# Kernel tuning notes

Measured on AMD Instinct MI355X. Metric: run time of the kernel, lower is better.

## Reference

```python
import jax, jax.numpy as jnp
import numpy as np

N = 50000      # nodes
E = 800000     # edges
IN = 128       # in_channels
H = 128        # hidden_channels
OUT = 500      # out_channels
EPS = 1e-5


def setup_inputs() -> dict:
    key = jax.random.key(0)
    ks = jax.random.split(key, 8)
    def rn(k, shape, scale=0.05):
        return jax.random.normal(k, shape, jnp.float32) * scale
    return {
        "x": jax.random.normal(ks[0], (N, IN), jnp.float32),
        "edge_index": jax.random.randint(ks[1], (2, E), 0, N, dtype=jnp.int32),
        "W1": rn(ks[2], (IN, H)), "b1": jnp.zeros((H,), jnp.float32),
        "g1": jnp.ones((H,), jnp.float32), "be1": jnp.zeros((H,), jnp.float32),
        "W2": rn(ks[3], (H, 2 * H)), "b2": jnp.zeros((2 * H,), jnp.float32),
        "g2": jnp.ones((2 * H,), jnp.float32), "be2": jnp.zeros((2 * H,), jnp.float32),
        "W3": rn(ks[4], (2 * H, H)), "b3": jnp.zeros((H,), jnp.float32),
        "g3": jnp.ones((H,), jnp.float32), "be3": jnp.zeros((H,), jnp.float32),
        "Wl1": rn(ks[5], (H, H // 2)), "bl1": jnp.zeros((H // 2,), jnp.float32),
        "g4": jnp.ones((H // 2,), jnp.float32), "be4": jnp.zeros((H // 2,), jnp.float32),
        "Wl2": rn(ks[6], (H // 2, OUT)), "bl2": jnp.zeros((OUT,), jnp.float32),
    }


def layer_norm(x, g, b):
    mu = jnp.mean(x, axis=-1, keepdims=True)
    var = jnp.mean(jnp.square(x - mu), axis=-1, keepdims=True)
    return (x - mu) * jax.lax.rsqrt(var + EPS) * g + b


def gcn_conv(x, W, b, src, dst, n):
    # PyG GCNConv: x' = D^{-1/2} (A + I) D^{-1/2} (x W) + b, with self-loops.
    h = x @ W                                   # [N, F]
    ones = jnp.ones(src.shape[0], h.dtype)
    deg = jax.ops.segment_sum(ones, dst, num_segments=n) + 1.0  # +1 self-loop
    dinv = jnp.where(deg > 0, jax.lax.rsqrt(deg), 0.0)          # [N]
    coef = dinv[src] * dinv[dst]                # [E]
    agg = jax.ops.segment_sum(h[src] * coef[:, None], dst, num_segments=n)
    agg = agg + h * jnp.square(dinv)[:, None]   # self-loop messages
    return agg + b


def reference(x, edge_index, W1, b1, g1, be1, W2, b2, g2, be2,
              W3, b3, g3, be3, Wl1, bl1, g4, be4, Wl2, bl2):
    # eval mode: dropout is identity
    src, dst = edge_index[0], edge_index[1]
    n = x.shape[0]
    h = jax.nn.elu(layer_norm(gcn_conv(x, W1, b1, src, dst, n), g1, be1))
    h = jax.nn.elu(layer_norm(gcn_conv(h, W2, b2, src, dst, n), g2, be2))
    h = jax.nn.elu(layer_norm(gcn_conv(h, W3, b3, src, dst, n), g3, be3))
    h = jax.nn.elu(layer_norm(h @ Wl1 + bl1, g4, be4))
    return h @ Wl2 + bl2
```

## Files before the change

kernel.cpp:

```cpp
#include <hip/hip_runtime.h>
#include <cstdint>


#define LN_EPS 1e-5f

typedef __attribute__((ext_vector_type(8))) short bf16x8;
typedef __attribute__((ext_vector_type(4))) float f32x4;

static __device__ __forceinline__ ushort f2bf(float f) {
  union { float f; uint u; } c; c.f = f;
  uint u = c.u;
  return (ushort)((u + 0x7fffu + ((u >> 16) & 1u)) >> 16);
}
static __device__ __forceinline__ float bf2f(ushort h) {
  union { uint u; float f; } c; c.u = (uint)h << 16;
  return c.f;
}


__global__ void zero2_kernel(int* __restrict__ a, int* __restrict__ b, int n) {
  int i = blockIdx.x * blockDim.x + threadIdx.x;
  if (i < n) { a[i] = 0; b[i] = 0; }
}

__global__ void deg_kernel(const int* __restrict__ dst, int* __restrict__ deg, int E) {
  int e = blockIdx.x * blockDim.x + threadIdx.x;
  if (e < E) atomicAdd(&deg[dst[e]], 1);
}

__global__ void scan1_kernel(const int* __restrict__ deg, int* __restrict__ excl,
                             int* __restrict__ bsums, float* __restrict__ dinv, int N) {
  __shared__ int s[256];
  int tid = threadIdx.x;
  int i = blockIdx.x * 256 + tid;
  int v = (i < N) ? deg[i] : 0;
  s[tid] = v;
  __syncthreads();
  for (int o = 1; o < 256; o <<= 1) {
    int t = (tid >= o) ? s[tid - o] : 0;
    __syncthreads();
    if (tid >= o) s[tid] += t;
    __syncthreads();
  }
  if (i < N) {
    excl[i] = s[tid] - v;
    dinv[i] = rsqrtf((float)v + 1.0f);
  }
  if (tid == 255) bsums[blockIdx.x] = s[tid];
}

__global__ void scan2_kernel(int* __restrict__ bsums, int nb) {
  __shared__ int s[256];
  int tid = threadIdx.x;
  int v = (tid < nb) ? bsums[tid] : 0;
  s[tid] = v;
  __syncthreads();
  for (int o = 1; o < 256; o <<= 1) {
    int t = (tid >= o) ? s[tid - o] : 0;
    __syncthreads();
    if (tid >= o) s[tid] += t;
    __syncthreads();
  }
  if (tid < nb) bsums[tid] = s[tid] - v;
}

__global__ void scan3_kernel(int* __restrict__ rowptr, const int* __restrict__ bsums,
                             int N, int Etotal) {
  int i = blockIdx.x * blockDim.x + threadIdx.x;
  if (i < N) rowptr[i] += bsums[i >> 8];
  else if (i == N) rowptr[N] = Etotal;
}

__global__ void fill_kernel(const int* __restrict__ src, const int* __restrict__ dst,
                            const int* __restrict__ rowptr, int* __restrict__ fill,
                            const float* __restrict__ dinv, int* __restrict__ srcs,
                            float* __restrict__ coefs, int E) {
  int e = blockIdx.x * blockDim.x + threadIdx.x;
  if (e >= E) return;
  int d = dst[e];
  int s = src[e];
  int pos = atomicAdd(&fill[d], 1);
  int idx = rowptr[d] + pos;
  srcs[idx] = s;
  coefs[idx] = dinv[s] * dinv[d];
}


__global__ void f2bf_vec_kernel(const float* __restrict__ in, ushort* __restrict__ out, int n4) {
  int i = blockIdx.x * blockDim.x + threadIdx.x;
  if (i >= n4) return;
  float4 v = ((const float4*)in)[i];
  ushort4 o;
  o.x = f2bf(v.x); o.y = f2bf(v.y); o.z = f2bf(v.z); o.w = f2bf(v.w);
  ((ushort4*)out)[i] = o;
}

struct WConvArgs {
  const float* w[5];
  ushort* wt[5];
  int K[5], N[5];
  int off[6];
};

__global__ void wconv_kernel(WConvArgs a, int total) {
  int i = blockIdx.x * blockDim.x + threadIdx.x;
  if (i >= total) return;
  int m = 0;
  while (i >= a.off[m + 1]) m++;
  int j = i - a.off[m];
  int k = j / a.N[m], n = j - k * a.N[m];
  a.wt[m][(size_t)n * a.K[m] + k] = f2bf(a.w[m][j]);
}

#define TBM 128
#define TBN 128
#define TBK 32
#define LDK 40

template <bool OUT_BF16>
__global__ __launch_bounds__(256, 2) void mfma_gemm_kernel(
    const ushort* __restrict__ A, const ushort* __restrict__ Bt,
    const float* __restrict__ bias, void* __restrict__ Cout,
    int M, int N, int K) {
  __shared__ ushort As[TBM][LDK];
  __shared__ ushort Bs[TBN][LDK];
  const int tid = threadIdx.x;
  const int lane = tid & 63;
  const int w = tid >> 6;
  const int wm = w & 1, wn = w >> 1;
  const int quad = lane >> 4, l16 = lane & 15;
  const int rowBase = blockIdx.y * TBM;
  const int colBase = blockIdx.x * TBN;

  f32x4 acc[4][4] = {};
  const int lr = tid >> 2;
  const int lk = (tid & 3) * 8;

  for (int k0 = 0; k0 < K; k0 += TBK) {
#pragma unroll
    for (int h = 0; h < 2; h++) {
      int r = lr + h * 64;
      int grow = rowBase + r;
      uint4 va = make_uint4(0, 0, 0, 0);
      if (grow < M) va = *(const uint4*)(A + (size_t)grow * K + k0 + lk);
      *(uint4*)&As[r][lk] = va;
      int gcol = colBase + r;
      uint4 vb = make_uint4(0, 0, 0, 0);
      if (gcol < N) vb = *(const uint4*)(Bt + (size_t)gcol * K + k0 + lk);
      *(uint4*)&Bs[r][lk] = vb;
    }
    __syncthreads();
    bf16x8 af[4], bfr[4];
#pragma unroll
    for (int i = 0; i < 4; i++) {
      af[i]  = *(const bf16x8*)&As[wm * 64 + i * 16 + l16][quad * 8];
      bfr[i] = *(const bf16x8*)&Bs[wn * 64 + i * 16 + l16][quad * 8];
    }
#pragma unroll
    for (int i = 0; i < 4; i++)
#pragma unroll
      for (int j = 0; j < 4; j++)
        acc[i][j] = __builtin_amdgcn_mfma_f32_16x16x32_bf16(af[i], bfr[j], acc[i][j], 0, 0, 0);
    __syncthreads();
  }
#pragma unroll
  for (int i = 0; i < 4; i++) {
    int row0 = rowBase + wm * 64 + i * 16 + quad * 4;
#pragma unroll
    for (int j = 0; j < 4; j++) {
      int col = colBase + wn * 64 + j * 16 + l16;
      if (col >= N) continue;
      float bv = bias ? bias[col] : 0.f;
#pragma unroll
      for (int r = 0; r < 4; r++) {
        int row = row0 + r;
        if (row >= M) continue;
        float v = acc[i][j][r] + bv;
        if (OUT_BF16) ((ushort*)Cout)[(size_t)row * N + col] = f2bf(v);
        else          ((float*)Cout)[(size_t)row * N + col] = v;
      }
    }
  }
}

template <bool OUT_BF16>
__global__ __launch_bounds__(256) void agg_kernel(
    const ushort* __restrict__ hb, const int* __restrict__ rowptr,
    const int* __restrict__ srcs, const float* __restrict__ coefs,
    const float* __restrict__ dinv, const float* __restrict__ bias,
    void* __restrict__ out, int Nn) {
  const int wave = threadIdx.x >> 6;
  const int n = blockIdx.x * 4 + wave;
  if (n >= Nn) return;
  const int f = threadIdx.x & 63;
  const uint* h32 = (const uint*)hb;
  const float di = dinv[n];
  uint self = h32[(size_t)n * 64 + f];
  float a0 = bf2f((ushort)(self & 0xffffu)) * di * di;
  float a1 = bf2f((ushort)(self >> 16)) * di * di;
  if (bias) { a0 += bias[2 * f]; a1 += bias[2 * f + 1]; }
  int i = rowptr[n];
  const int e = rowptr[n + 1];
  for (; i + 3 < e; i += 4) {
    int s0 = srcs[i], s1 = srcs[i + 1], s2 = srcs[i + 2], s3 = srcs[i + 3];
    float c0 = coefs[i], c1 = coefs[i + 1], c2 = coefs[i + 2], c3 = coefs[i + 3];
    uint v0 = h32[(size_t)s0 * 64 + f];
    uint v1 = h32[(size_t)s1 * 64 + f];
    uint v2 = h32[(size_t)s2 * 64 + f];
    uint v3 = h32[(size_t)s3 * 64 + f];
    a0 += c0 * bf2f((ushort)(v0 & 0xffffu)) + c1 * bf2f((ushort)(v1 & 0xffffu)) +
          c2 * bf2f((ushort)(v2 & 0xffffu)) + c3 * bf2f((ushort)(v3 & 0xffffu));
    a1 += c0 * bf2f((ushort)(v0 >> 16)) + c1 * bf2f((ushort)(v1 >> 16)) +
          c2 * bf2f((ushort)(v2 >> 16)) + c3 * bf2f((ushort)(v3 >> 16));
  }
  for (; i < e; i++) {
    float c = coefs[i];
    uint v = h32[(size_t)srcs[i] * 64 + f];
    a0 += c * bf2f((ushort)(v & 0xffffu));
    a1 += c * bf2f((ushort)(v >> 16));
  }
  if (OUT_BF16) {
    uint o = (uint)f2bf(a0) | ((uint)f2bf(a1) << 16);
    ((uint*)out)[(size_t)n * 64 + f] = o;
  } else {
    ((float2*)out)[(size_t)n * 64 + f] = make_float2(a0, a1);
  }
}

template <int F, bool IN_BF16>
__global__ __launch_bounds__(F) void ln_elu_kernel(const void* __restrict__ xin,
                                                   const float* __restrict__ g,
                                                   const float* __restrict__ be,
                                                   ushort* __restrict__ out) {
  constexpr int NW = (F + 63) / 64;
  __shared__ float sb[NW];
  const int row = blockIdx.x;
  const int f = threadIdx.x;
  float v;
  if (IN_BF16) v = bf2f(((const ushort*)xin)[(size_t)row * F + f]);
  else         v = ((const float*)xin)[(size_t)row * F + f];
  float s = v;
#pragma unroll
  for (int o = 32; o >= 1; o >>= 1) s += __shfl_xor(s, o);
  float mean;
  if constexpr (NW == 1) {
    mean = s * (1.0f / F);
  } else {
    if ((f & 63) == 0) sb[f >> 6] = s;
    __syncthreads();
    float t = 0.f;
#pragma unroll
    for (int w2 = 0; w2 < NW; w2++) t += sb[w2];
    mean = t * (1.0f / F);
    __syncthreads();
  }
  float d = v - mean;
  float q = d * d;
#pragma unroll
  for (int o = 32; o >= 1; o >>= 1) q += __shfl_xor(q, o);
  float var;
  if constexpr (NW == 1) {
    var = q * (1.0f / F);
  } else {
    if ((f & 63) == 0) sb[f >> 6] = q;
    __syncthreads();
    float t = 0.f;
#pragma unroll
    for (int w2 = 0; w2 < NW; w2++) t += sb[w2];
    var = t * (1.0f / F);
  }
  float y = d * rsqrtf(var + LN_EPS) * g[f] + be[f];
  out[(size_t)row * F + f] = f2bf((y > 0.f) ? y : expm1f(y));
}


extern "C" void kernel_launch(void* const* d_in, const int* in_sizes, int n_in,
                              void* d_out, int out_size, void* d_ws, size_t ws_size,
                              hipStream_t stream) {
  const float* x   = (const float*)d_in[0];
  const int*   ei  = (const int*)d_in[1];
  const float* W1  = (const float*)d_in[2];
  const float* b1  = (const float*)d_in[3];
  const float* g1  = (const float*)d_in[4];
  const float* be1 = (const float*)d_in[5];
  const float* W2  = (const float*)d_in[6];
  const float* b2  = (const float*)d_in[7];
  const float* g2  = (const float*)d_in[8];
  const float* be2 = (const float*)d_in[9];
  const float* W3  = (const float*)d_in[10];
  const float* b3  = (const float*)d_in[11];
  const float* g3  = (const float*)d_in[12];
  const float* be3 = (const float*)d_in[13];
  const float* Wl1 = (const float*)d_in[14];
  const float* bl1 = (const float*)d_in[15];
  const float* g4  = (const float*)d_in[16];
  const float* be4 = (const float*)d_in[17];
  const float* Wl2 = (const float*)d_in[18];
  const float* bl2 = (const float*)d_in[19];

  const int N = in_sizes[0] / 128;
  const int E = in_sizes[1] / 2;
  const int* esrc = ei;
  const int* edst = ei + E;

  char* p = (char*)d_ws;
  float* F1 = (float*)p;              p += (size_t)N * 128 * 4;
  ushort* Pb = (ushort*)p;            p += (size_t)N * 256 * 2;
  ushort* Qb = (ushort*)p;            p += (size_t)N * 256 * 2;
  ushort* W1t = (ushort*)p;           p += 128 * 128 * 2;
  ushort* W2t = (ushort*)p;           p += 128 * 256 * 2;
  ushort* W3t = (ushort*)p;           p += 256 * 128 * 2;
  ushort* Wl1t = (ushort*)p;          p += 128 * 64 * 2;
  ushort* Wl2t = (ushort*)p;          p += 64 * 500 * 2;
  int*   srcs  = (int*)p;             p += (size_t)E * 4;
  float* coefs = (float*)p;           p += (size_t)E * 4;
  int*   deg   = (int*)p;             p += (size_t)N * 4;
  float* dinv  = (float*)p;           p += (size_t)N * 4;
  int*   rowptr= (int*)p;             p += (size_t)(N + 2) * 4;
  int*   fill  = (int*)p;             p += (size_t)N * 4;
  int*   bsums = (int*)p;             p += 256 * 4;
  ushort* xb = (ushort*)F1;

  const int nb = (N + 255) / 256;
  const int eb = (E + 255) / 256;

  zero2_kernel<<<nb, 256, 0, stream>>>(deg, fill, N);
  deg_kernel<<<eb, 256, 0, stream>>>(edst, deg, E);
  scan1_kernel<<<nb, 256, 0, stream>>>(deg, rowptr, bsums, dinv, N);
  scan2_kernel<<<1, 256, 0, stream>>>(bsums, nb);
  scan3_kernel<<<(N + 256) / 256, 256, 0, stream>>>(rowptr, bsums, N, E);
  fill_kernel<<<eb, 256, 0, stream>>>(esrc, edst, rowptr, fill, dinv, srcs, coefs, E);

  f2bf_vec_kernel<<<(N * 128 / 4 + 255) / 256, 256, 0, stream>>>(x, xb, N * 128 / 4);
  WConvArgs wa;
  wa.w[0] = W1;  wa.wt[0] = W1t;  wa.K[0] = 128; wa.N[0] = 128;
  wa.w[1] = W2;  wa.wt[1] = W2t;  wa.K[1] = 128; wa.N[1] = 256;
  wa.w[2] = W3;  wa.wt[2] = W3t;  wa.K[2] = 256; wa.N[2] = 128;
  wa.w[3] = Wl1; wa.wt[3] = Wl1t; wa.K[3] = 128; wa.N[3] = 64;
  wa.w[4] = Wl2; wa.wt[4] = Wl2t; wa.K[4] = 64;  wa.N[4] = 500;
  wa.off[0] = 0;
  for (int m = 0; m < 5; m++) wa.off[m + 1] = wa.off[m] + wa.K[m] * wa.N[m];
  int wtotal = wa.off[5];
  wconv_kernel<<<(wtotal + 255) / 256, 256, 0, stream>>>(wa, wtotal);

  auto gemm_bf = [&](const ushort* A, const ushort* Bt, const float* bias, ushort* C,
                     int M, int Nn, int K) {
    dim3 grid((Nn + TBN - 1) / TBN, (M + TBM - 1) / TBM);
    mfma_gemm_kernel<true><<<grid, 256, 0, stream>>>(A, Bt, bias, C, M, Nn, K);
  };
  auto gemm_f32 = [&](const ushort* A, const ushort* Bt, const float* bias, float* C,
                      int M, int Nn, int K) {
    dim3 grid((Nn + TBN - 1) / TBN, (M + TBM - 1) / TBM);
    mfma_gemm_kernel<false><<<grid, 256, 0, stream>>>(A, Bt, bias, C, M, Nn, K);
  };
  const int ab = (N + 3) / 4;

  gemm_bf(xb, W1t, nullptr, Pb, N, 128, 128);
  agg_kernel<false><<<ab, 256, 0, stream>>>(Pb, rowptr, srcs, coefs, dinv, b1, F1, N);
  ln_elu_kernel<128, false><<<N, 128, 0, stream>>>(F1, g1, be1, Qb);

  agg_kernel<true><<<ab, 256, 0, stream>>>(Qb, rowptr, srcs, coefs, dinv, nullptr, Pb, N);
  gemm_bf(Pb, W2t, b2, Qb, N, 256, 128);
  ln_elu_kernel<256, true><<<N, 256, 0, stream>>>(Qb, g2, be2, Pb);

  gemm_bf(Pb, W3t, nullptr, Qb, N, 128, 256);
  agg_kernel<false><<<ab, 256, 0, stream>>>(Qb, rowptr, srcs, coefs, dinv, b3, F1, N);
  ln_elu_kernel<128, false><<<N, 128, 0, stream>>>(F1, g3, be3, Pb);

  gemm_f32(Pb, Wl1t, bl1, F1, N, 64, 128);
  ln_elu_kernel<64, false><<<N, 64, 0, stream>>>(F1, g4, be4, Qb);

  gemm_f32(Qb, Wl2t, bl2, (float*)d_out, N, 500, 64);
}
```

Measured before the change: 575.3 us.

## Fuse GCN aggregation with LayerNorm+ELU and compute edge coefficients on the fly

Layers 1 and 3 now do aggregation, bias, LayerNorm and ELU in a single wave-per-node kernel that writes bf16 output. This removes the fp32 intermediate round trip and two ln_elu launches. The per-edge coefficient array is dropped: coefficients are computed from dinv of the source times dinv of the destination inside aggregation, which costs an extra gather of dinv per edge in exchange for less CSR build traffic. The fill counters are also seeded with rowptr in scan3, so the fill kernel no longer needs a separate zeroing pass or the rowptr lookup.

```diff
diff --git a/kernel.cpp b/kernel.cpp
--- a/kernel.cpp
+++ b/kernel.cpp
@@ -18,9 +18,9 @@
 }
 
 
-__global__ void zero2_kernel(int* __restrict__ a, int* __restrict__ b, int n) {
+__global__ void zero1_kernel(int* __restrict__ a, int n) {
   int i = blockIdx.x * blockDim.x + threadIdx.x;
-  if (i < n) { a[i] = 0; b[i] = 0; }
+  if (i < n) a[i] = 0;
 }
 
 __global__ void deg_kernel(const int* __restrict__ dst, int* __restrict__ deg, int E) {
@@ -64,25 +64,24 @@
   if (tid < nb) bsums[tid] = s[tid] - v;
 }
 
-__global__ void scan3_kernel(int* __restrict__ rowptr, const int* __restrict__ bsums,
-                             int N, int Etotal) {
+__global__ void scan3_kernel(int* __restrict__ rowptr, int* __restrict__ fill,
+                             const int* __restrict__ bsums, int N, int Etotal) {
   int i = blockIdx.x * blockDim.x + threadIdx.x;
-  if (i < N) rowptr[i] += bsums[i >> 8];
-  else if (i == N) rowptr[N] = Etotal;
+  if (i < N) {
+    int v = rowptr[i] + bsums[i >> 8];
+    rowptr[i] = v;
+    fill[i] = v;
+  } else if (i == N) {
+    rowptr[N] = Etotal;
+  }
 }
 
 __global__ void fill_kernel(const int* __restrict__ src, const int* __restrict__ dst,
-                            const int* __restrict__ rowptr, int* __restrict__ fill,
-                            const float* __restrict__ dinv, int* __restrict__ srcs,
-                            float* __restrict__ coefs, int E) {
+                            int* __restrict__ fill, int* __restrict__ srcs, int E) {
   int e = blockIdx.x * blockDim.x + threadIdx.x;
   if (e >= E) return;
-  int d = dst[e];
-  int s = src[e];
-  int pos = atomicAdd(&fill[d], 1);
-  int idx = rowptr[d] + pos;
-  srcs[idx] = s;
-  coefs[idx] = dinv[s] * dinv[d];
+  int idx = atomicAdd(&fill[dst[e]], 1);
+  srcs[idx] = src[e];
 }
 
 
@@ -183,12 +182,11 @@
   }
 }
 
-template <bool OUT_BF16>
+
 __global__ __launch_bounds__(256) void agg_kernel(
     const ushort* __restrict__ hb, const int* __restrict__ rowptr,
-    const int* __restrict__ srcs, const float* __restrict__ coefs,
-    const float* __restrict__ dinv, const float* __restrict__ bias,
-    void* __restrict__ out, int Nn) {
+    const int* __restrict__ srcs, const float* __restrict__ dinv,
+    uint* __restrict__ out, int Nn) {
   const int wave = threadIdx.x >> 6;
   const int n = blockIdx.x * 4 + wave;
   if (n >= Nn) return;
@@ -198,12 +196,11 @@
   uint self = h32[(size_t)n * 64 + f];
   float a0 = bf2f((ushort)(self & 0xffffu)) * di * di;
   float a1 = bf2f((ushort)(self >> 16)) * di * di;
-  if (bias) { a0 += bias[2 * f]; a1 += bias[2 * f + 1]; }
   int i = rowptr[n];
   const int e = rowptr[n + 1];
   for (; i + 3 < e; i += 4) {
     int s0 = srcs[i], s1 = srcs[i + 1], s2 = srcs[i + 2], s3 = srcs[i + 3];
-    float c0 = coefs[i], c1 = coefs[i + 1], c2 = coefs[i + 2], c3 = coefs[i + 3];
+    float c0 = dinv[s0] * di, c1 = dinv[s1] * di, c2 = dinv[s2] * di, c3 = dinv[s3] * di;
     uint v0 = h32[(size_t)s0 * 64 + f];
     uint v1 = h32[(size_t)s1 * 64 + f];
     uint v2 = h32[(size_t)s2 * 64 + f];
@@ -214,17 +211,67 @@
           c2 * bf2f((ushort)(v2 >> 16)) + c3 * bf2f((ushort)(v3 >> 16));
   }
   for (; i < e; i++) {
-    float c = coefs[i];
-    uint v = h32[(size_t)srcs[i] * 64 + f];
+    int s = srcs[i];
+    float c = dinv[s] * di;
+    uint v = h32[(size_t)s * 64 + f];
     a0 += c * bf2f((ushort)(v & 0xffffu));
     a1 += c * bf2f((ushort)(v >> 16));
   }
-  if (OUT_BF16) {
-    uint o = (uint)f2bf(a0) | ((uint)f2bf(a1) << 16);
-    ((uint*)out)[(size_t)n * 64 + f] = o;
-  } else {
-    ((float2*)out)[(size_t)n * 64 + f] = make_float2(a0, a1);
-  }
+  out[(size_t)n * 64 + f] = (uint)f2bf(a0) | ((uint)f2bf(a1) << 16);
+}
+
+__global__ __launch_bounds__(256) void agg_ln_kernel(
+    const ushort* __restrict__ hb, const int* __restrict__ rowptr,
+    const int* __restrict__ srcs, const float* __restrict__ dinv,
+    const float* __restrict__ bias, const float* __restrict__ g,
+    const float* __restrict__ be, uint* __restrict__ out, int Nn) {
+  const int wave = threadIdx.x >> 6;
+  const int n = blockIdx.x * 4 + wave;
+  if (n >= Nn) return;
+  const int f = threadIdx.x & 63;
+  const uint* h32 = (const uint*)hb;
+  const float di = dinv[n];
+  uint self = h32[(size_t)n * 64 + f];
+  float2 bv = ((const float2*)bias)[f];
+  float a0 = bf2f((ushort)(self & 0xffffu)) * di * di + bv.x;
+  float a1 = bf2f((ushort)(self >> 16)) * di * di + bv.y;
+  int i = rowptr[n];
+  const int e = rowptr[n + 1];
+  for (; i + 3 < e; i += 4) {
+    int s0 = srcs[i], s1 = srcs[i + 1], s2 = srcs[i + 2], s3 = srcs[i + 3];
+    float c0 = dinv[s0] * di, c1 = dinv[s1] * di, c2 = dinv[s2] * di, c3 = dinv[s3] * di;
+    uint v0 = h32[(size_t)s0 * 64 + f];
+    uint v1 = h32[(size_t)s1 * 64 + f];
+    uint v2 = h32[(size_t)s2 * 64 + f];
+    uint v3 = h32[(size_t)s3 * 64 + f];
+    a0 += c0 * bf2f((ushort)(v0 & 0xffffu)) + c1 * bf2f((ushort)(v1 & 0xffffu)) +
+          c2 * bf2f((ushort)(v2 & 0xffffu)) + c3 * bf2f((ushort)(v3 & 0xffffu));
+    a1 += c0 * bf2f((ushort)(v0 >> 16)) + c1 * bf2f((ushort)(v1 >> 16)) +
+          c2 * bf2f((ushort)(v2 >> 16)) + c3 * bf2f((ushort)(v3 >> 16));
+  }
+  for (; i < e; i++) {
+    int s = srcs[i];
+    float c = dinv[s] * di;
+    uint v = h32[(size_t)s * 64 + f];
+    a0 += c * bf2f((ushort)(v & 0xffffu));
+    a1 += c * bf2f((ushort)(v >> 16));
+  }
+  float s = a0 + a1;
+#pragma unroll
+  for (int o = 32; o >= 1; o >>= 1) s += __shfl_xor(s, o);
+  float mean = s * (1.0f / 128.0f);
+  float d0 = a0 - mean, d1 = a1 - mean;
+  float q = d0 * d0 + d1 * d1;
+#pragma unroll
+  for (int o = 32; o >= 1; o >>= 1) q += __shfl_xor(q, o);
+  float rstd = rsqrtf(q * (1.0f / 128.0f) + LN_EPS);
+  float2 gv = ((const float2*)g)[f];
+  float2 bev = ((const float2*)be)[f];
+  float y0 = d0 * rstd * gv.x + bev.x;
+  float y1 = d1 * rstd * gv.y + bev.y;
+  y0 = (y0 > 0.f) ? y0 : expm1f(y0);
+  y1 = (y1 > 0.f) ? y1 : expm1f(y1);
+  out[(size_t)n * 64 + f] = (uint)f2bf(y0) | ((uint)f2bf(y1) << 16);
 }
 
 template <int F, bool IN_BF16>
@@ -313,7 +360,6 @@
   ushort* Wl1t = (ushort*)p;          p += 128 * 64 * 2;
   ushort* Wl2t = (ushort*)p;          p += 64 * 500 * 2;
   int*   srcs  = (int*)p;             p += (size_t)E * 4;
-  float* coefs = (float*)p;           p += (size_t)E * 4;
   int*   deg   = (int*)p;             p += (size_t)N * 4;
   float* dinv  = (float*)p;           p += (size_t)N * 4;
   int*   rowptr= (int*)p;             p += (size_t)(N + 2) * 4;
@@ -324,12 +370,12 @@
   const int nb = (N + 255) / 256;
   const int eb = (E + 255) / 256;
 
-  zero2_kernel<<<nb, 256, 0, stream>>>(deg, fill, N);
+  zero1_kernel<<<nb, 256, 0, stream>>>(deg, N);
   deg_kernel<<<eb, 256, 0, stream>>>(edst, deg, E);
   scan1_kernel<<<nb, 256, 0, stream>>>(deg, rowptr, bsums, dinv, N);
   scan2_kernel<<<1, 256, 0, stream>>>(bsums, nb);
-  scan3_kernel<<<(N + 256) / 256, 256, 0, stream>>>(rowptr, bsums, N, E);
-  fill_kernel<<<eb, 256, 0, stream>>>(esrc, edst, rowptr, fill, dinv, srcs, coefs, E);
+  scan3_kernel<<<(N + 256) / 256, 256, 0, stream>>>(rowptr, fill, bsums, N, E);
+  fill_kernel<<<eb, 256, 0, stream>>>(esrc, edst, fill, srcs, E);
 
   f2bf_vec_kernel<<<(N * 128 / 4 + 255) / 256, 256, 0, stream>>>(x, xb, N * 128 / 4);
   WConvArgs wa;
@@ -356,16 +402,14 @@
   const int ab = (N + 3) / 4;
 
   gemm_bf(xb, W1t, nullptr, Pb, N, 128, 128);
-  agg_kernel<false><<<ab, 256, 0, stream>>>(Pb, rowptr, srcs, coefs, dinv, b1, F1, N);
-  ln_elu_kernel<128, false><<<N, 128, 0, stream>>>(F1, g1, be1, Qb);
-
-  agg_kernel<true><<<ab, 256, 0, stream>>>(Qb, rowptr, srcs, coefs, dinv, nullptr, Pb, N);
+  agg_ln_kernel<<<ab, 256, 0, stream>>>(Pb, rowptr, srcs, dinv, b1, g1, be1, (uint*)Qb, N);
+
+  agg_kernel<<<ab, 256, 0, stream>>>(Qb, rowptr, srcs, dinv, (uint*)Pb, N);
   gemm_bf(Pb, W2t, b2, Qb, N, 256, 128);
   ln_elu_kernel<256, true><<<N, 256, 0, stream>>>(Qb, g2, be2, Pb);
 
   gemm_bf(Pb, W3t, nullptr, Qb, N, 128, 256);
-  agg_kernel<false><<<ab, 256, 0, stream>>>(Qb, rowptr, srcs, coefs, dinv, b3, F1, N);
-  ln_elu_kernel<128, false><<<N, 128, 0, stream>>>(F1, g3, be3, Pb);
+  agg_ln_kernel<<<ab, 256, 0, stream>>>(Qb, rowptr, srcs, dinv, b3, g3, be3, (uint*)Pb, N);
 
   gemm_f32(Pb, Wl1t, bl1, F1, N, 64, 128);
   ln_elu_kernel<64, false><<<N, 64, 0, stream>>>(F1, g4, be4, Qb);
```

After: 529.7 us. 7.9% less time.
